# Kernel optimization log

Measured on AMD Instinct MI355X. Metric: run time of the kernel, lower is better.

The kernel has to match this reference:

```python
import jax, jax.numpy as jnp
import numpy as np

NUM_HEADS = 8
HEAD_DIM = 64
EPS = 1e-4

def _act(x):
    # 1 + elu(x) == where(x > 0, x + 1, exp(x))
    return jnp.where(x > 0, x + 1.0, jnp.exp(x))

def setup_inputs() -> dict:
    key = jax.random.key(0)
    k1, k2, k3 = jax.random.split(key, 3)
    b, n, dim = 16, 4096, 512
    inner = NUM_HEADS * HEAD_DIM
    x = jax.random.normal(k1, (b, n, dim), dtype=jnp.float32)
    W_qkv = jax.random.normal(k2, (3 * inner, dim), dtype=jnp.float32) * (dim ** -0.5)
    W_out = jax.random.normal(k3, (dim, inner), dtype=jnp.float32) * (inner ** -0.5)
    b_out = jnp.zeros((dim,), dtype=jnp.float32)
    return {"x": x, "W_qkv": W_qkv, "W_out": W_out, "b_out": b_out}

def reference(x, W_qkv, W_out, b_out):
    b, n, dim = x.shape
    inner = NUM_HEADS * HEAD_DIM
    qkv = x @ W_qkv.T                                     # [b, n, 3*inner]
    q, k, v = jnp.split(qkv, 3, axis=-1)
    def to_heads(t):
        return t.reshape(b, n, NUM_HEADS, HEAD_DIM).transpose(0, 2, 1, 3)  # [b, h, n, d]
    q, k, v = to_heads(q), to_heads(k), to_heads(v)
    q = _act(q)
    k = _act(k)
    # kv = sum_n k_n (outer) v_n  -> [b, h, d, e]
    kv = jnp.einsum('bhnd,bhne->bhde', k, v)
    # denominator: q . sum_n k_n, clamped at eps
    k_sum = k.sum(axis=-2)                                # [b, h, d]
    z = 1.0 / jnp.maximum(jnp.einsum('bhnd,bhd->bhn', q, k_sum), EPS)
    out = jnp.einsum('bhnd,bhde,bhn->bhne', q, kv, z)     # [b, h, n, e]
    out = out.transpose(0, 2, 1, 3).reshape(b, n, inner)  # [b, n, h*d]
    return out @ W_out.T + b_out
```

## Files before the change

kernel.cpp:

```cpp
#include <hip/hip_runtime.h>


typedef unsigned short u16;
typedef u16 u16x4 __attribute__((ext_vector_type(4)));
typedef u16 u16x8 __attribute__((ext_vector_type(8)));
typedef __bf16 bf16x8 __attribute__((ext_vector_type(8)));
typedef float f32x4 __attribute__((ext_vector_type(4)));

__device__ __forceinline__ u16 f2bf(float f) {
    union { float f; unsigned u; } t; t.f = f;
    unsigned r = t.u + 0x7fffu + ((t.u >> 16) & 1u);
    return (u16)(r >> 16);
}
__device__ __forceinline__ float act_fn(float v) {
    return v > 0.0f ? v + 1.0f : __expf(v);
}
__device__ __forceinline__ void cvt8(const float* __restrict__ s, u16* __restrict__ d) {
    f32x4 lo = *(const f32x4*)s;
    f32x4 hi = *(const f32x4*)(s + 4);
    u16x8 o = { f2bf(lo[0]), f2bf(lo[1]), f2bf(lo[2]), f2bf(lo[3]),
                f2bf(hi[0]), f2bf(hi[1]), f2bf(hi[2]), f2bf(hi[3]) };
    *(u16x8*)d = o;
}
__device__ __forceinline__ void gld16(const u16* g, u16* l) {
    __builtin_amdgcn_global_load_lds(
        (__attribute__((address_space(1))) const void*)g,
        (__attribute__((address_space(3))) void*)l, 16, 0, 0);
}

__global__ __launch_bounds__(256) void convert_all(const float* __restrict__ x,
                                                   const float* __restrict__ Wqkv,
                                                   const float* __restrict__ Wout,
                                                   u16* __restrict__ xb,
                                                   u16* __restrict__ wq,
                                                   u16* __restrict__ wo,
                                                   float* __restrict__ kvg)
{
    size_t u = (size_t)blockIdx.x * 256 + threadIdx.x;
    if (u < 4194304ull) {
        cvt8(x + u * 8, xb + u * 8);
    } else if (u < 4292608ull) {
        u -= 4194304ull;
        const int drow = (int)(u >> 6);
        int srow;
        if (drow < 512) srow = drow;
        else {
            const int t = drow - 512, h = t >> 7, j = t & 127;
            srow = (j < 64) ? (512 + h * 64 + j) : (1024 + h * 64 + (j - 64));
        }
        cvt8(Wqkv + (size_t)srow * 512 + (u & 63) * 8, wq + u * 8);
    } else if (u < 4325376ull) {
        u -= 4292608ull; cvt8(Wout + u * 8, wo + u * 8);
    } else {
        u -= 4325376ull;
        f32x4 z = { 0.f, 0.f, 0.f, 0.f };
        *(f32x4*)&kvg[u * 8] = z;
        *(f32x4*)&kvg[u * 8 + 4] = z;
    }
}

__global__ __launch_bounds__(256) void gemm_qkv(const u16* __restrict__ A,
                                                const u16* __restrict__ Bw,
                                                u16* __restrict__ Cq,
                                                float* __restrict__ kvglob)
{
    __shared__ u16 SMF[16384];
    const int nt = blockIdx.x;
    const int mt = blockIdx.y;
    const size_t row0 = (size_t)mt * 128;
    const int col0 = nt * 128;
    const int tid = threadIdx.x, wave = tid >> 6, lane = tid & 63;
    const int frow = lane & 15, quad = lane >> 4;
    const int wr = (wave >> 1) * 64, wc = (wave & 1) * 64;

    f32x4 acc[4][4] = {};

    const int ch0 = wave * 64 + lane, ch1 = 256 + ch0;
    const int r0 = ch0 >> 2, c0 = (ch0 & 3) * 8;
    const int r1 = ch1 >> 2, c1 = (ch1 & 3) * 8;
    const u16* gA0 = A + (row0 + r0) * 512 + c0;
    const u16* gA1 = A + (row0 + r1) * 512 + c1;
    const u16* gB0 = Bw + (size_t)(col0 + r0) * 512 + c0;
    const u16* gB1 = Bw + (size_t)(col0 + r1) * 512 + c1;

#define QKV_STAGE(buf, k0) do {                                   \
        u16* As_ = SMF + (buf) * 8192;                            \
        u16* Bs_ = As_ + 4096;                                    \
        gld16(gA0 + (k0), As_ + wave * 512);                      \
        gld16(gA1 + (k0), As_ + 2048 + wave * 512);               \
        gld16(gB0 + (k0), Bs_ + wave * 512);                      \
        gld16(gB1 + (k0), Bs_ + 2048 + wave * 512);               \
    } while (0)

    QKV_STAGE(0, 0);
    __syncthreads();
    int cur = 0;
    for (int t = 0; t < 16; ++t) {
        if (t < 15) QKV_STAGE(cur ^ 1, (t + 1) * 32);
        const u16* As_ = SMF + cur * 8192;
        const u16* Bs_ = As_ + 4096;
        bf16x8 af[4], bfr[4];
#pragma unroll
        for (int mi = 0; mi < 4; ++mi)
            af[mi] = *(const bf16x8*)&As_[(wr + mi * 16 + frow) * 32 + quad * 8];
#pragma unroll
        for (int ni = 0; ni < 4; ++ni)
            bfr[ni] = *(const bf16x8*)&Bs_[(wc + ni * 16 + frow) * 32 + quad * 8];
#pragma unroll
        for (int mi = 0; mi < 4; ++mi)
#pragma unroll
            for (int ni = 0; ni < 4; ++ni)
                acc[mi][ni] = __builtin_amdgcn_mfma_f32_16x16x32_bf16(af[mi], bfr[ni], acc[mi][ni], 0, 0, 0);
        __syncthreads();
        cur ^= 1;
    }
#undef QKV_STAGE

    if (col0 < 512) {
#pragma unroll
        for (int mi = 0; mi < 4; ++mi) {
#pragma unroll
            for (int ni = 0; ni < 4; ++ni) {
                const int c = col0 + wc + ni * 16 + frow;
                const size_t rbase = row0 + wr + mi * 16 + quad * 4;
#pragma unroll
                for (int reg = 0; reg < 4; ++reg)
                    Cq[(rbase + reg) * 512 + c] = f2bf(act_fn(acc[mi][ni][reg]));
            }
        }
        return;
    }

    u16* KT = SMF;
    u16* VT = SMF + 4608;
    for (int i = tid; i < 16 * 72; i += 256)
        VT[64 * 72 + i] = (i < 64) ? (u16)0x3F80 : (u16)0;

    const bool is_k = (wc == 0);
    f32x4 kvacc[5] = {};

#pragma unroll
    for (int half = 0; half < 2; ++half) {
        __syncthreads();
        if ((wave >> 1) == half) {
#pragma unroll
            for (int mi = 0; mi < 4; ++mi) {
                const int n0 = wr + mi * 16 + quad * 4 - half * 64;
#pragma unroll
                for (int ni = 0; ni < 4; ++ni) {
                    const int cl = wc + ni * 16 + frow;
                    u16x4 o;
#pragma unroll
                    for (int reg = 0; reg < 4; ++reg) {
                        float v = acc[mi][ni][reg];
                        if (is_k) v = act_fn(v);
                        o[reg] = f2bf(v);
                    }
                    if (is_k) *(u16x4*)&KT[cl * 72 + n0] = o;
                    else      *(u16x4*)&VT[(cl - 64) * 72 + n0] = o;
                }
            }
        }
        __syncthreads();
#pragma unroll
        for (int c = 0; c < 2; ++c) {
            bf16x8 af2 = *(const bf16x8*)&KT[(wave * 16 + frow) * 72 + c * 32 + quad * 8];
#pragma unroll
            for (int et = 0; et < 5; ++et) {
                bf16x8 bf2 = *(const bf16x8*)&VT[(et * 16 + frow) * 72 + c * 32 + quad * 8];
                kvacc[et] = __builtin_amdgcn_mfma_f32_16x16x32_bf16(af2, bf2, kvacc[et], 0, 0, 0);
            }
        }
    }

    const int b = mt >> 5, h = nt - 4;
    float* dst = kvglob + (size_t)(b * 8 + h) * 5120;
#pragma unroll
    for (int et = 0; et < 5; ++et) {
        const int e = et * 16 + frow;
        if (e <= 64) {
#pragma unroll
            for (int reg = 0; reg < 4; ++reg) {
                const int d = wave * 16 + quad * 4 + reg;
                atomicAdd(&dst[d * 80 + e], kvacc[et][reg]);
            }
        }
    }
}

__global__ __launch_bounds__(256) void reduce_kvt(const float* __restrict__ kvglob,
                                                  u16* __restrict__ kvt)
{
    const int bh = blockIdx.x, tid = threadIdx.x;
    for (int i = tid; i < 5120; i += 256) {
        const int e = i >> 6, d = i & 63;
        kvt[(size_t)bh * 5120 + i] =
            (e < 65) ? f2bf(kvglob[(size_t)bh * 5120 + d * 80 + e]) : (u16)0;
    }
}

__global__ __launch_bounds__(256) void apply_attn(u16* __restrict__ qio,
                                                  const u16* __restrict__ kvt)
{
    const int blk = blockIdx.x;
    const size_t t0 = (size_t)blk * 128;
    const int bb = blk >> 5;
    const int tid = threadIdx.x, wave = tid >> 6, lane = tid & 63;
    const int frow = lane & 15, quad = lane >> 4;
    const int wt = wave * 32;
    const int h0 = blockIdx.y * 2;

    for (int h = h0; h < h0 + 2; ++h) {
        const u16* kvh = kvt + (size_t)(bb * 8 + h) * 5120;
        f32x4 acc[5][2] = {};
#pragma unroll
        for (int kc = 0; kc < 2; ++kc) {
            bf16x8 bfr[2];
#pragma unroll
            for (int ni = 0; ni < 2; ++ni)
                bfr[ni] = *(const bf16x8*)&qio[(t0 + wt + ni * 16 + frow) * 512 + h * 64 + kc * 32 + quad * 8];
#pragma unroll
            for (int mi = 0; mi < 5; ++mi) {
                bf16x8 afr = *(const bf16x8*)&kvh[(mi * 16 + frow) * 64 + kc * 32 + quad * 8];
#pragma unroll
                for (int ni = 0; ni < 2; ++ni)
                    acc[mi][ni] = __builtin_amdgcn_mfma_f32_16x16x32_bf16(afr, bfr[ni], acc[mi][ni], 0, 0, 0);
            }
        }
#pragma unroll
        for (int ni = 0; ni < 2; ++ni) {
            const float den = __shfl(acc[4][ni][0], frow, 64);
            const float z = 1.0f / fmaxf(den, 1e-4f);
            const size_t tok = t0 + wt + ni * 16 + frow;
#pragma unroll
            for (int mi = 0; mi < 4; ++mi) {
                u16x4 o;
#pragma unroll
                for (int reg = 0; reg < 4; ++reg) o[reg] = f2bf(acc[mi][ni][reg] * z);
                *(u16x4*)&qio[tok * 512 + h * 64 + mi * 16 + quad * 4] = o;
            }
        }
    }
}

__global__ __launch_bounds__(256) void gemm_out(const u16* __restrict__ A,
                                                const u16* __restrict__ Bw,
                                                float* __restrict__ C,
                                                const float* __restrict__ bias)
{
    __shared__ u16 SMF[16384];
    const int nt = blockIdx.x;
    const int mt = blockIdx.y;
    const size_t row0 = (size_t)mt * 128;
    const int col0 = nt * 128;
    const int tid  = threadIdx.x;
    const int wave = tid >> 6, lane = tid & 63;
    const int wr = (wave >> 1) * 64, wc = (wave & 1) * 64;
    const int frow = lane & 15, quad = lane >> 4;

    f32x4 acc[4][4] = {};

    const int ch0 = wave * 64 + lane, ch1 = 256 + ch0;
    const int r0 = ch0 >> 2, c0 = (ch0 & 3) * 8;
    const int r1 = ch1 >> 2, c1 = (ch1 & 3) * 8;
    const u16* gA0 = A + (row0 + r0) * 512 + c0;
    const u16* gA1 = A + (row0 + r1) * 512 + c1;
    const u16* gB0 = Bw + (size_t)(col0 + r0) * 512 + c0;
    const u16* gB1 = Bw + (size_t)(col0 + r1) * 512 + c1;

#define OUT_STAGE(buf, k0) do {                                   \
        u16* As_ = SMF + (buf) * 8192;                            \
        u16* Bs_ = As_ + 4096;                                    \
        gld16(gA0 + (k0), As_ + wave * 512);                      \
        gld16(gA1 + (k0), As_ + 2048 + wave * 512);               \
        gld16(gB0 + (k0), Bs_ + wave * 512);                      \
        gld16(gB1 + (k0), Bs_ + 2048 + wave * 512);               \
    } while (0)

    OUT_STAGE(0, 0);
    __syncthreads();
    int cur = 0;
    for (int t = 0; t < 16; ++t) {
        if (t < 15) OUT_STAGE(cur ^ 1, (t + 1) * 32);
        const u16* As_ = SMF + cur * 8192;
        const u16* Bs_ = As_ + 4096;
        bf16x8 af[4], bfr[4];
#pragma unroll
        for (int mi = 0; mi < 4; ++mi)
            af[mi] = *(const bf16x8*)&As_[(wr + mi * 16 + frow) * 32 + quad * 8];
#pragma unroll
        for (int ni = 0; ni < 4; ++ni)
            bfr[ni] = *(const bf16x8*)&Bs_[(wc + ni * 16 + frow) * 32 + quad * 8];
#pragma unroll
        for (int mi = 0; mi < 4; ++mi)
#pragma unroll
            for (int ni = 0; ni < 4; ++ni)
                acc[mi][ni] = __builtin_amdgcn_mfma_f32_16x16x32_bf16(af[mi], bfr[ni], acc[mi][ni], 0, 0, 0);
        __syncthreads();
        cur ^= 1;
    }
#undef OUT_STAGE

#pragma unroll
    for (int mi = 0; mi < 4; ++mi) {
#pragma unroll
        for (int ni = 0; ni < 4; ++ni) {
            const int c = col0 + wc + ni * 16 + frow;
            const float bv = bias[c];
            const size_t rbase = row0 + wr + mi * 16 + quad * 4;
#pragma unroll
            for (int reg = 0; reg < 4; ++reg)
                C[(rbase + reg) * 512 + c] = acc[mi][ni][reg] + bv;
        }
    }
}

extern "C" void kernel_launch(void* const* d_in, const int* in_sizes, int n_in,
                              void* d_out, int out_size, void* d_ws, size_t ws_size,
                              hipStream_t stream)
{
    const float* x    = (const float*)d_in[0];
    const float* Wqkv = (const float*)d_in[1];
    const float* Wout = (const float*)d_in[2];
    const float* bout = (const float*)d_in[3];
    float* out = (float*)d_out;
    char* ws = (char*)d_ws;

    u16*   wq_bf  = (u16*)ws;
    u16*   wo_bf  = (u16*)(ws + 1572864ull);
    u16*   wsq    = (u16*)(ws + 2097152ull);
    u16*   xb     = (u16*)(ws + 69206016ull);
    float* kvglob = (float*)(ws + 136314880ull);
    u16*   kvt    = (u16*)(ws + 138936320ull);

    convert_all<<<17216, 256, 0, stream>>>(x, Wqkv, Wout, xb, wq_bf, wo_bf, kvglob);
    gemm_qkv<<<dim3(12, 512), 256, 0, stream>>>(xb, wq_bf, wsq, kvglob);
    reduce_kvt<<<128, 256, 0, stream>>>(kvglob, kvt);
    apply_attn<<<dim3(512, 4), 256, 0, stream>>>(wsq, kvt);
    gemm_out<<<dim3(4, 512), 256, 0, stream>>>(wsq, wo_bf, out, bout);
}
```

Measured before the change: 490.1 us.

## Fuse attention apply into output projection GEMM and remap block order

Merges apply_attn and gemm_out into one kernel. Each block computes the normalized attention output for its 128 tokens one head at a time into LDS and immediately multiplies it by the matching W_out slice, accumulating the output tile in registers. This removes the bf16 write and re-read of the attention output through global memory and one kernel launch. In exchange, each of the 4 column tiles recomputes the q·kv product, and W_out is read directly from global without LDS staging. Both GEMM kernels also get a block-id swizzle that interleaves blocks in groups of 8, presumably to change cache locality.

```diff
diff --git a/kernel.cpp b/kernel.cpp
--- a/kernel.cpp
+++ b/kernel.cpp
@@ -65,8 +65,10 @@
                                                 float* __restrict__ kvglob)
 {
     __shared__ u16 SMF[16384];
-    const int nt = blockIdx.x;
-    const int mt = blockIdx.y;
+    const int id = blockIdx.y * 12 + blockIdx.x;
+    const int o  = (id & 7) * 768 + (id >> 3);
+    const int nt = o % 12;
+    const int mt = o / 12;
     const size_t row0 = (size_t)mt * 128;
     const int col0 = nt * 128;
     const int tid = threadIdx.x, wave = tid >> 6, lane = tid & 63;
@@ -149,15 +151,15 @@
 #pragma unroll
                 for (int ni = 0; ni < 4; ++ni) {
                     const int cl = wc + ni * 16 + frow;
-                    u16x4 o;
+                    u16x4 o2;
 #pragma unroll
                     for (int reg = 0; reg < 4; ++reg) {
                         float v = acc[mi][ni][reg];
                         if (is_k) v = act_fn(v);
-                        o[reg] = f2bf(v);
+                        o2[reg] = f2bf(v);
                     }
-                    if (is_k) *(u16x4*)&KT[cl * 72 + n0] = o;
-                    else      *(u16x4*)&VT[(cl - 64) * 72 + n0] = o;
+                    if (is_k) *(u16x4*)&KT[cl * 72 + n0] = o2;
+                    else      *(u16x4*)&VT[(cl - 64) * 72 + n0] = o2;
                 }
             }
         }
@@ -199,18 +201,27 @@
     }
 }
 
-__global__ __launch_bounds__(256) void apply_attn(u16* __restrict__ qio,
-                                                  const u16* __restrict__ kvt)
-{
-    const int blk = blockIdx.x;
-    const size_t t0 = (size_t)blk * 128;
-    const int bb = blk >> 5;
+__global__ __launch_bounds__(256) void fused_out(const u16* __restrict__ Q,
+                                                 const u16* __restrict__ kvt,
+                                                 const u16* __restrict__ Bw,
+                                                 float* __restrict__ C,
+                                                 const float* __restrict__ bias)
+{
+    __shared__ u16 attnL[128 * 72];
+    const int id = blockIdx.y * 4 + blockIdx.x;
+    const int o  = (id & 7) * 256 + (id >> 3);
+    const int nt = o & 3, mt = o >> 2;
+    const size_t t0 = (size_t)mt * 128;
+    const int col0 = nt * 128;
+    const int bb = mt >> 5;
     const int tid = threadIdx.x, wave = tid >> 6, lane = tid & 63;
     const int frow = lane & 15, quad = lane >> 4;
     const int wt = wave * 32;
-    const int h0 = blockIdx.y * 2;
-
-    for (int h = h0; h < h0 + 2; ++h) {
+    const int wr = (wave >> 1) * 64, wc = (wave & 1) * 64;
+
+    f32x4 oacc[4][4] = {};
+
+    for (int h = 0; h < 8; ++h) {
         const u16* kvh = kvt + (size_t)(bb * 8 + h) * 5120;
         f32x4 acc[5][2] = {};
 #pragma unroll
@@ -218,7 +229,7 @@
             bf16x8 bfr[2];
 #pragma unroll
             for (int ni = 0; ni < 2; ++ni)
-                bfr[ni] = *(const bf16x8*)&qio[(t0 + wt + ni * 16 + frow) * 512 + h * 64 + kc * 32 + quad * 8];
+                bfr[ni] = *(const bf16x8*)&Q[(t0 + wt + ni * 16 + frow) * 512 + h * 64 + kc * 32 + quad * 8];
 #pragma unroll
             for (int mi = 0; mi < 5; ++mi) {
                 bf16x8 afr = *(const bf16x8*)&kvh[(mi * 16 + frow) * 64 + kc * 32 + quad * 8];
@@ -227,79 +238,37 @@
                     acc[mi][ni] = __builtin_amdgcn_mfma_f32_16x16x32_bf16(afr, bfr[ni], acc[mi][ni], 0, 0, 0);
             }
         }
+        __syncthreads();
 #pragma unroll
         for (int ni = 0; ni < 2; ++ni) {
             const float den = __shfl(acc[4][ni][0], frow, 64);
             const float z = 1.0f / fmaxf(den, 1e-4f);
-            const size_t tok = t0 + wt + ni * 16 + frow;
+            const int tok = wt + ni * 16 + frow;
 #pragma unroll
             for (int mi = 0; mi < 4; ++mi) {
-                u16x4 o;
-#pragma unroll
-                for (int reg = 0; reg < 4; ++reg) o[reg] = f2bf(acc[mi][ni][reg] * z);
-                *(u16x4*)&qio[tok * 512 + h * 64 + mi * 16 + quad * 4] = o;
-            }
-        }
-    }
-}
-
-__global__ __launch_bounds__(256) void gemm_out(const u16* __restrict__ A,
-                                                const u16* __restrict__ Bw,
-                                                float* __restrict__ C,
-                                                const float* __restrict__ bias)
-{
-    __shared__ u16 SMF[16384];
-    const int nt = blockIdx.x;
-    const int mt = blockIdx.y;
-    const size_t row0 = (size_t)mt * 128;
-    const int col0 = nt * 128;
-    const int tid  = threadIdx.x;
-    const int wave = tid >> 6, lane = tid & 63;
-    const int wr = (wave >> 1) * 64, wc = (wave & 1) * 64;
-    const int frow = lane & 15, quad = lane >> 4;
-
-    f32x4 acc[4][4] = {};
-
-    const int ch0 = wave * 64 + lane, ch1 = 256 + ch0;
-    const int r0 = ch0 >> 2, c0 = (ch0 & 3) * 8;
-    const int r1 = ch1 >> 2, c1 = (ch1 & 3) * 8;
-    const u16* gA0 = A + (row0 + r0) * 512 + c0;
-    const u16* gA1 = A + (row0 + r1) * 512 + c1;
-    const u16* gB0 = Bw + (size_t)(col0 + r0) * 512 + c0;
-    const u16* gB1 = Bw + (size_t)(col0 + r1) * 512 + c1;
-
-#define OUT_STAGE(buf, k0) do {                                   \
-        u16* As_ = SMF + (buf) * 8192;                            \
-        u16* Bs_ = As_ + 4096;                                    \
-        gld16(gA0 + (k0), As_ + wave * 512);                      \
-        gld16(gA1 + (k0), As_ + 2048 + wave * 512);               \
-        gld16(gB0 + (k0), Bs_ + wave * 512);                      \
-        gld16(gB1 + (k0), Bs_ + 2048 + wave * 512);               \
-    } while (0)
-
-    OUT_STAGE(0, 0);
-    __syncthreads();
-    int cur = 0;
-    for (int t = 0; t < 16; ++t) {
-        if (t < 15) OUT_STAGE(cur ^ 1, (t + 1) * 32);
-        const u16* As_ = SMF + cur * 8192;
-        const u16* Bs_ = As_ + 4096;
-        bf16x8 af[4], bfr[4];
-#pragma unroll
-        for (int mi = 0; mi < 4; ++mi)
-            af[mi] = *(const bf16x8*)&As_[(wr + mi * 16 + frow) * 32 + quad * 8];
-#pragma unroll
-        for (int ni = 0; ni < 4; ++ni)
-            bfr[ni] = *(const bf16x8*)&Bs_[(wc + ni * 16 + frow) * 32 + quad * 8];
-#pragma unroll
-        for (int mi = 0; mi < 4; ++mi)
+                u16x4 t;
+#pragma unroll
+                for (int reg = 0; reg < 4; ++reg) t[reg] = f2bf(acc[mi][ni][reg] * z);
+                *(u16x4*)&attnL[tok * 72 + mi * 16 + quad * 4] = t;
+            }
+        }
+        __syncthreads();
+#pragma unroll
+        for (int kk = 0; kk < 2; ++kk) {
+            bf16x8 af[4], bfr2[4];
+#pragma unroll
+            for (int mi = 0; mi < 4; ++mi)
+                af[mi] = *(const bf16x8*)&attnL[(wr + mi * 16 + frow) * 72 + kk * 32 + quad * 8];
 #pragma unroll
             for (int ni = 0; ni < 4; ++ni)
-                acc[mi][ni] = __builtin_amdgcn_mfma_f32_16x16x32_bf16(af[mi], bfr[ni], acc[mi][ni], 0, 0, 0);
-        __syncthreads();
-        cur ^= 1;
-    }
-#undef OUT_STAGE
+                bfr2[ni] = *(const bf16x8*)&Bw[(size_t)(col0 + wc + ni * 16 + frow) * 512 + h * 64 + kk * 32 + quad * 8];
+#pragma unroll
+            for (int mi = 0; mi < 4; ++mi)
+#pragma unroll
+                for (int ni = 0; ni < 4; ++ni)
+                    oacc[mi][ni] = __builtin_amdgcn_mfma_f32_16x16x32_bf16(af[mi], bfr2[ni], oacc[mi][ni], 0, 0, 0);
+        }
+    }
 
 #pragma unroll
     for (int mi = 0; mi < 4; ++mi) {
@@ -307,10 +276,10 @@
         for (int ni = 0; ni < 4; ++ni) {
             const int c = col0 + wc + ni * 16 + frow;
             const float bv = bias[c];
-            const size_t rbase = row0 + wr + mi * 16 + quad * 4;
+            const size_t rbase = t0 + wr + mi * 16 + quad * 4;
 #pragma unroll
             for (int reg = 0; reg < 4; ++reg)
-                C[(rbase + reg) * 512 + c] = acc[mi][ni][reg] + bv;
+                C[(rbase + reg) * 512 + c] = oacc[mi][ni][reg] + bv;
         }
     }
 }
@@ -336,6 +305,5 @@
     convert_all<<<17216, 256, 0, stream>>>(x, Wqkv, Wout, xb, wq_bf, wo_bf, kvglob);
     gemm_qkv<<<dim3(12, 512), 256, 0, stream>>>(xb, wq_bf, wsq, kvglob);
     reduce_kvt<<<128, 256, 0, stream>>>(kvglob, kvt);
-    apply_attn<<<dim3(512, 4), 256, 0, stream>>>(wsq, kvt);
-    gemm_out<<<dim3(4, 512), 256, 0, stream>>>(wsq, wo_bf, out, bout);
-}
+    fused_out<<<dim3(4, 512), 256, 0, stream>>>(wsq, kvt, wo_bf, out, bout);
+}
```

Measured after the change: 553.9 us. 13.0% more time.

## Fold per-head kv matrix into output projection weights per batch

Applied to the files above, without the earlier changes.

Instead of computing q·kv per head and then multiplying by W_out, the kernel precomputes P_b = W_out·blockdiag(kv) per batch and applies the output GEMM directly on normalized q. The apply_attn MFMA pass becomes a lightweight elementwise normalization by the per-head denominator (apply_z), and the final GEMM reads a batch-specific weight matrix. This removes one full pass of small GEMMs over all tokens at the cost of an extra kernel building P and an additional bf16 rounding of P.

```diff
diff --git a/kernel.cpp b/kernel.cpp
--- a/kernel.cpp
+++ b/kernel.cpp
@@ -7,6 +7,9 @@
 typedef __bf16 bf16x8 __attribute__((ext_vector_type(8)));
 typedef float f32x4 __attribute__((ext_vector_type(4)));
 
+__device__ __forceinline__ float bf2f(u16 x) {
+    union { unsigned u; float f; } t; t.u = ((unsigned)x) << 16; return t.f;
+}
 __device__ __forceinline__ u16 f2bf(float f) {
     union { float f; unsigned u; } t; t.f = f;
     unsigned r = t.u + 0x7fffu + ((t.u >> 16) & 1u);
@@ -149,15 +152,15 @@
 #pragma unroll
                 for (int ni = 0; ni < 4; ++ni) {
                     const int cl = wc + ni * 16 + frow;
-                    u16x4 o;
+                    u16x4 o2;
 #pragma unroll
                     for (int reg = 0; reg < 4; ++reg) {
                         float v = acc[mi][ni][reg];
                         if (is_k) v = act_fn(v);
-                        o[reg] = f2bf(v);
+                        o2[reg] = f2bf(v);
                     }
-                    if (is_k) *(u16x4*)&KT[cl * 72 + n0] = o;
-                    else      *(u16x4*)&VT[(cl - 64) * 72 + n0] = o;
+                    if (is_k) *(u16x4*)&KT[cl * 72 + n0] = o2;
+                    else      *(u16x4*)&VT[(cl - 64) * 72 + n0] = o2;
                 }
             }
         }
@@ -188,71 +191,104 @@
     }
 }
 
-__global__ __launch_bounds__(256) void reduce_kvt(const float* __restrict__ kvglob,
-                                                  u16* __restrict__ kvt)
-{
-    const int bh = blockIdx.x, tid = threadIdx.x;
-    for (int i = tid; i < 5120; i += 256) {
-        const int e = i >> 6, d = i & 63;
-        kvt[(size_t)bh * 5120 + i] =
-            (e < 65) ? f2bf(kvglob[(size_t)bh * 5120 + d * 80 + e]) : (u16)0;
-    }
-}
-
-__global__ __launch_bounds__(256) void apply_attn(u16* __restrict__ qio,
-                                                  const u16* __restrict__ kvt)
-{
-    const int blk = blockIdx.x;
-    const size_t t0 = (size_t)blk * 128;
-    const int bb = blk >> 5;
+__global__ __launch_bounds__(256) void make_P(const float* __restrict__ kvglob,
+                                              const u16* __restrict__ wo,
+                                              u16* __restrict__ P,
+                                              u16* __restrict__ ksum)
+{
+    __shared__ u16 kvb[64 * 72];
+    const int bh = blockIdx.x, b = bh >> 3, h = bh & 7;
     const int tid = threadIdx.x, wave = tid >> 6, lane = tid & 63;
     const int frow = lane & 15, quad = lane >> 4;
-    const int wt = wave * 32;
-    const int h0 = blockIdx.y * 2;
-
-    for (int h = h0; h < h0 + 2; ++h) {
-        const u16* kvh = kvt + (size_t)(bb * 8 + h) * 5120;
-        f32x4 acc[5][2] = {};
-#pragma unroll
-        for (int kc = 0; kc < 2; ++kc) {
-            bf16x8 bfr[2];
-#pragma unroll
-            for (int ni = 0; ni < 2; ++ni)
-                bfr[ni] = *(const bf16x8*)&qio[(t0 + wt + ni * 16 + frow) * 512 + h * 64 + kc * 32 + quad * 8];
-#pragma unroll
-            for (int mi = 0; mi < 5; ++mi) {
-                bf16x8 afr = *(const bf16x8*)&kvh[(mi * 16 + frow) * 64 + kc * 32 + quad * 8];
-#pragma unroll
-                for (int ni = 0; ni < 2; ++ni)
-                    acc[mi][ni] = __builtin_amdgcn_mfma_f32_16x16x32_bf16(afr, bfr[ni], acc[mi][ni], 0, 0, 0);
-            }
-        }
-#pragma unroll
-        for (int ni = 0; ni < 2; ++ni) {
-            const float den = __shfl(acc[4][ni][0], frow, 64);
-            const float z = 1.0f / fmaxf(den, 1e-4f);
-            const size_t tok = t0 + wt + ni * 16 + frow;
-#pragma unroll
-            for (int mi = 0; mi < 4; ++mi) {
-                u16x4 o;
-#pragma unroll
-                for (int reg = 0; reg < 4; ++reg) o[reg] = f2bf(acc[mi][ni][reg] * z);
-                *(u16x4*)&qio[tok * 512 + h * 64 + mi * 16 + quad * 4] = o;
-            }
-        }
-    }
-}
-
-__global__ __launch_bounds__(256) void gemm_out(const u16* __restrict__ A,
-                                                const u16* __restrict__ Bw,
-                                                float* __restrict__ C,
-                                                const float* __restrict__ bias)
+    const float* src = kvglob + (size_t)bh * 5120;
+
+    for (int i = tid; i < 4096; i += 256)
+        kvb[(i >> 6) * 72 + (i & 63)] = f2bf(src[(i >> 6) * 80 + (i & 63)]);
+    if (tid < 64) ksum[bh * 64 + tid] = f2bf(src[tid * 80 + 64]);
+    __syncthreads();
+
+    f32x4 acc[8][4] = {};
+    const int m0 = wave * 128;
+#pragma unroll
+    for (int k2 = 0; k2 < 2; ++k2) {
+        bf16x8 bfr[4];
+#pragma unroll
+        for (int ni = 0; ni < 4; ++ni)
+            bfr[ni] = *(const bf16x8*)&kvb[(ni * 16 + frow) * 72 + k2 * 32 + quad * 8];
+#pragma unroll
+        for (int mi = 0; mi < 8; ++mi) {
+            bf16x8 af = *(const bf16x8*)&wo[(size_t)(m0 + mi * 16 + frow) * 512 + h * 64 + k2 * 32 + quad * 8];
+#pragma unroll
+            for (int ni = 0; ni < 4; ++ni)
+                acc[mi][ni] = __builtin_amdgcn_mfma_f32_16x16x32_bf16(af, bfr[ni], acc[mi][ni], 0, 0, 0);
+        }
+    }
+
+    u16* Pb = P + (size_t)b * 262144;
+#pragma unroll
+    for (int mi = 0; mi < 8; ++mi) {
+#pragma unroll
+        for (int ni = 0; ni < 4; ++ni) {
+            const int d = ni * 16 + frow;
+#pragma unroll
+            for (int reg = 0; reg < 4; ++reg) {
+                const int c = m0 + mi * 16 + quad * 4 + reg;
+                Pb[(size_t)c * 512 + h * 64 + d] = f2bf(acc[mi][ni][reg]);
+            }
+        }
+    }
+}
+
+__global__ __launch_bounds__(256) void apply_z(u16* __restrict__ qio,
+                                               const u16* __restrict__ ksum)
+{
+    const int g = blockIdx.x * 256 + threadIdx.x;
+    const int tok = g >> 2, p = g & 3;
+    const int b = tok >> 12;
+    u16* qrow = qio + (size_t)tok * 512 + p * 128;
+    const u16* ks = ksum + b * 512 + p * 128;
+
+    u16x8 q[16];
+    float den[2] = { 0.f, 0.f };
+#pragma unroll
+    for (int half = 0; half < 2; ++half) {
+#pragma unroll
+        for (int jj = 0; jj < 8; ++jj) {
+            const int idx = half * 8 + jj;
+            q[idx] = *(const u16x8*)&qrow[idx * 8];
+            u16x8 k8 = *(const u16x8*)&ks[idx * 8];
+#pragma unroll
+            for (int e = 0; e < 8; ++e)
+                den[half] += bf2f(q[idx][e]) * bf2f(k8[e]);
+        }
+    }
+    const float z0 = 1.0f / fmaxf(den[0], 1e-4f);
+    const float z1 = 1.0f / fmaxf(den[1], 1e-4f);
+#pragma unroll
+    for (int half = 0; half < 2; ++half) {
+        const float z = half ? z1 : z0;
+#pragma unroll
+        for (int jj = 0; jj < 8; ++jj) {
+            const int idx = half * 8 + jj;
+            u16x8 o;
+#pragma unroll
+            for (int e = 0; e < 8; ++e) o[e] = f2bf(bf2f(q[idx][e]) * z);
+            *(u16x8*)&qrow[idx * 8] = o;
+        }
+    }
+}
+
+__global__ __launch_bounds__(256) void gemm_final(const u16* __restrict__ A,
+                                                  const u16* __restrict__ P,
+                                                  float* __restrict__ C,
+                                                  const float* __restrict__ bias)
 {
     __shared__ u16 SMF[16384];
     const int nt = blockIdx.x;
     const int mt = blockIdx.y;
     const size_t row0 = (size_t)mt * 128;
     const int col0 = nt * 128;
+    const u16* Bw = P + (size_t)(mt >> 5) * 262144;
     const int tid  = threadIdx.x;
     const int wave = tid >> 6, lane = tid & 63;
     const int wr = (wave >> 1) * 64, wc = (wave & 1) * 64;
@@ -330,12 +366,13 @@
     u16*   wo_bf  = (u16*)(ws + 1572864ull);
     u16*   wsq    = (u16*)(ws + 2097152ull);
     u16*   xb     = (u16*)(ws + 69206016ull);
+    u16*   P      = xb;
     float* kvglob = (float*)(ws + 136314880ull);
-    u16*   kvt    = (u16*)(ws + 138936320ull);
+    u16*   ksum   = (u16*)(ws + 138936320ull);
 
     convert_all<<<17216, 256, 0, stream>>>(x, Wqkv, Wout, xb, wq_bf, wo_bf, kvglob);
     gemm_qkv<<<dim3(12, 512), 256, 0, stream>>>(xb, wq_bf, wsq, kvglob);
-    reduce_kvt<<<128, 256, 0, stream>>>(kvglob, kvt);
-    apply_attn<<<dim3(512, 4), 256, 0, stream>>>(wsq, kvt);
-    gemm_out<<<dim3(4, 512), 256, 0, stream>>>(wsq, wo_bf, out, bout);
-}
+    make_P<<<128, 256, 0, stream>>>(kvglob, wo_bf, P, ksum);
+    apply_z<<<1024, 256, 0, stream>>>(wsq, ksum);
+    gemm_final<<<dim3(4, 512), 256, 0, stream>>>(wsq, P, out, bout);
+}
```

Result: slower. 508.9 us (+3.8%).
